# Kernel tuning notes

Measured on AMD Instinct MI355X. Metric: run time of the kernel, lower is better.

Reference implementation:

```python
import jax, jax.numpy as jnp
import numpy as np

N = 100000      # nodes
E = 1600000     # edges (avg degree 16)
F_IN = 128      # node feature dim
HID = 128       # conv1 out
EMB = 64        # conv2 out (embedding)
OUT = 40        # classes


def setup_inputs() -> dict:
    key = jax.random.key(0)
    ks = jax.random.split(key, 8)
    x = jax.random.normal(ks[0], (N, F_IN), dtype=jnp.float32)
    edge_index = jax.random.randint(ks[1], (2, E), 0, N, dtype=jnp.int64)

    def glorot(k, shape):
        lim = np.sqrt(6.0 / (shape[0] + shape[1])).astype(np.float32)
        return jax.random.uniform(k, shape, jnp.float32, -lim, lim)

    W1 = glorot(ks[2], (F_IN, HID)); b1 = jnp.zeros((HID,), jnp.float32)
    W2 = glorot(ks[3], (HID, EMB)); b2 = jnp.zeros((EMB,), jnp.float32)
    Wl = glorot(ks[4], (EMB, OUT)); bl = jnp.zeros((OUT,), jnp.float32)
    return {"x": x, "edge_index": edge_index,
            "W1": W1, "b1": b1, "W2": W2, "b2": b2, "Wl": Wl, "bl": bl}


def _gcn_conv(x, W, b, src, dst, norm, n):
    # GCNConv: linear transform first (smaller width earlier), then normalized
    # sparse aggregation: out_i = sum_{j->i} norm_e * (x_j W) + b
    h = x @ W
    out = jax.ops.segment_sum(h[src] * norm[:, None], dst, num_segments=n)
    return out + b


def reference(x, edge_index, W1, b1, W2, b2, Wl, bl):
    n = x.shape[0]
    loop = jnp.arange(n, dtype=edge_index.dtype)
    # add self loops (GCNConv default)
    src = jnp.concatenate([edge_index[0], loop])
    dst = jnp.concatenate([edge_index[1], loop])
    # symmetric degree normalization: D^{-1/2} (A+I) D^{-1/2}
    deg = jax.ops.segment_sum(jnp.ones_like(dst, x.dtype), dst, num_segments=n)
    dinv = jnp.where(deg > 0, jax.lax.rsqrt(deg), 0.0)
    norm = dinv[src] * dinv[dst]

    h = jax.nn.relu(_gcn_conv(x, W1, b1, src, dst, norm, n))
    # F.dropout(training=False) is identity in eval mode
    embedding = _gcn_conv(h, W2, b2, src, dst, norm, n)
    logits = embedding @ Wl + bl
    return jax.nn.log_softmax(logits, axis=1), embedding
```

## Files before the change

kernel.cpp:

```cpp
#include <hip/hip_runtime.h>
#include <math.h>

#define F_IN 128
#define HIDN 128
#define EMBD 64
#define OUTC 40

#define NBINS 1024
#define BIN_SHIFT 7
#define CSR_BLKS 256

__host__ __device__ static inline int imin(int a, int b) { return a < b ? a : b; }

typedef __attribute__((ext_vector_type(8))) short s16x8;
typedef __attribute__((ext_vector_type(4))) float f32x4;

__device__ __forceinline__ unsigned short f2bf(float f) {
    unsigned int u = __builtin_bit_cast(unsigned int, f);
    u = (u + 0x7FFFu + ((u >> 16) & 1u)) >> 16;
    return (unsigned short)u;
}
__device__ __forceinline__ float bflo(unsigned int v) {
    return __builtin_bit_cast(float, v << 16);
}
__device__ __forceinline__ float bfhi(unsigned int v) {
    return __builtin_bit_cast(float, v & 0xFFFF0000u);
}

__host__ __device__ static inline int csr_chunk(int E) {
    return (((E + CSR_BLKS - 1) / CSR_BLKS) + 3) & ~3;
}

__global__ __launch_bounds__(256) void prep_frags_kernel(
    const float* __restrict__ W1, const float* __restrict__ W2,
    const float* __restrict__ Wl, unsigned short* __restrict__ W1f,
    unsigned short* __restrict__ W2f, unsigned short* __restrict__ Wlf) {
    int s = blockIdx.x * 256 + threadIdx.x;
    if (s < 2048) {
        int lane = s & 63, r = s >> 6;
        int ks = r & 3, cf = (r >> 2) & 3, wcol = r >> 4;
        int c = wcol * 64 + cf * 16 + (lane & 15);
        int kb = ks * 32 + (lane >> 4) * 8;
        unsigned short* d = W1f + s * 8;
#pragma unroll
        for (int j = 0; j < 8; ++j) d[j] = f2bf(W1[(size_t)(kb + j) * HIDN + c]);
    } else if (s < 3072) {
        int q = s - 2048;
        int lane = q & 63, r = q >> 6;
        int ks = r & 3, wv = r >> 2;
        int c = wv * 16 + (lane & 15);
        int kb = ks * 32 + (lane >> 4) * 8;
        unsigned short* d = W2f + q * 8;
#pragma unroll
        for (int j = 0; j < 8; ++j) d[j] = f2bf(W2[(size_t)(kb + j) * EMBD + c]);
    } else if (s < 3456) {
        int q = s - 3072;
        int lane = q & 63, r = q >> 6;
        int ks = r & 1, ct = r >> 1;
        int c = ct * 16 + (lane & 15);
        int kb = ks * 32 + (lane >> 4) * 8;
        unsigned short* d = Wlf + q * 8;
#pragma unroll
        for (int j = 0; j < 8; ++j)
            d[j] = (c < OUTC) ? f2bf(Wl[(size_t)(kb + j) * OUTC + c]) : (unsigned short)0;
    }
}

__global__ __launch_bounds__(256) void coarse_hist_kernel(const int* __restrict__ dst,
                                                          int* __restrict__ bc, int E) {
    __shared__ int h[NBINS];
    for (int i = threadIdx.x; i < NBINS; i += 256) h[i] = 0;
    __syncthreads();
    const int chunk = csr_chunk(E);
    const int e0 = blockIdx.x * chunk;
    const int e1 = imin(e0 + chunk, E);
    for (int e = e0 + threadIdx.x; e < e1; e += 256)
        atomicAdd(&h[dst[e] >> BIN_SHIFT], 1);
    __syncthreads();
    for (int i = threadIdx.x; i < NBINS; i += 256)
        bc[blockIdx.x * NBINS + i] = h[i];
}

__global__ __launch_bounds__(64) void bin_prefix_kernel(int* __restrict__ bc,
                                                        int* __restrict__ bintot) {
    const int bin = blockIdx.x * 64 + threadIdx.x;
    int run = 0;
    for (int blk = 0; blk < CSR_BLKS; ++blk) {
        int v = bc[blk * NBINS + bin];
        bc[blk * NBINS + bin] = run;
        run += v;
    }
    bintot[bin] = run;
}

__global__ __launch_bounds__(1024) void bin_scan_kernel(const int* __restrict__ bintot,
                                                        int* __restrict__ cs) {
    __shared__ int s[NBINS];
    const int t = threadIdx.x;
    s[t] = bintot[t];
    __syncthreads();
    for (int off = 1; off < NBINS; off <<= 1) {
        int v = (t >= off) ? s[t - off] : 0;
        __syncthreads();
        s[t] += v;
        __syncthreads();
    }
    cs[t + 1] = s[t];
    if (t == 0) cs[0] = 0;
}

__global__ __launch_bounds__(256) void bin_scatter_kernel(const int* __restrict__ src,
                                                          const int* __restrict__ dst,
                                                          const int* __restrict__ bc,
                                                          const int* __restrict__ cs,
                                                          int* __restrict__ ebuf, int E) {
    __shared__ int cur[NBINS];
    for (int i = threadIdx.x; i < NBINS; i += 256)
        cur[i] = cs[i] + bc[blockIdx.x * NBINS + i];
    __syncthreads();
    const int chunk = csr_chunk(E);
    const int e0 = blockIdx.x * chunk;
    const int e1 = imin(e0 + chunk, E);
    int e = e0 + threadIdx.x * 4;
    for (; e + 3 < e1; e += 256 * 4) {
        int4 d = *(const int4*)(dst + e);
        int4 s = *(const int4*)(src + e);
        int p0 = atomicAdd(&cur[d.x >> BIN_SHIFT], 1);
        int p1 = atomicAdd(&cur[d.y >> BIN_SHIFT], 1);
        int p2 = atomicAdd(&cur[d.z >> BIN_SHIFT], 1);
        int p3 = atomicAdd(&cur[d.w >> BIN_SHIFT], 1);
        ebuf[p0] = (s.x << BIN_SHIFT) | (d.x & 127);
        ebuf[p1] = (s.y << BIN_SHIFT) | (d.y & 127);
        ebuf[p2] = (s.z << BIN_SHIFT) | (d.z & 127);
        ebuf[p3] = (s.w << BIN_SHIFT) | (d.w & 127);
    }
    for (; e < e1; ++e) {
        int d = dst[e];
        int pos = atomicAdd(&cur[d >> BIN_SHIFT], 1);
        ebuf[pos] = (src[e] << BIN_SHIFT) | (d & 127);
    }
}

__global__ __launch_bounds__(256) void fine_build_kernel(const int* __restrict__ ebuf,
                                                         const int* __restrict__ cs,
                                                         int* __restrict__ degi,
                                                         int* __restrict__ rowptr,
                                                         float* __restrict__ dinv,
                                                         int* __restrict__ col, int n) {
    __shared__ int h[128];
    __shared__ int fs[128];
    __shared__ int cur[128];
    const int b = blockIdx.x;
    const int node0 = b << BIN_SHIFT;
    const int t = threadIdx.x;
    if (t < 128) h[t] = 0;
    __syncthreads();
    const int e0 = cs[b], e1 = cs[b + 1];
    for (int e = e0 + t; e < e1; e += 256)
        atomicAdd(&h[ebuf[e] & 127], 1);
    __syncthreads();
    if (t < 128) fs[t] = h[t];
    __syncthreads();
    for (int off = 1; off < 128; off <<= 1) {
        int v = 0;
        if (t < 128 && t >= off) v = fs[t - off];
        __syncthreads();
        if (t < 128) fs[t] += v;
        __syncthreads();
    }
    if (t < 128) {
        int node = node0 + t;
        if (node < n) {
            int cnt = h[t];
            degi[node] = cnt;
            rowptr[node] = e0 + fs[t] - cnt;
            dinv[node] = rsqrtf((float)cnt + 1.0f);
        }
        cur[t] = 0;
    }
    __syncthreads();
    for (int e = e0 + t; e < e1; e += 256) {
        int p = ebuf[e];
        int li = p & 127;
        int loc = atomicAdd(&cur[li], 1);
        col[e0 + (fs[li] - h[li]) + loc] = p >> BIN_SHIFT;
    }
}

template <typename InT, int K, int M, int WM, int WN>
__global__ __launch_bounds__(256) void gemm_mfma_kernel(const InT* __restrict__ X,
                                                        const unsigned short* __restrict__ Wfrag,
                                                        const float* __restrict__ dinv,
                                                        unsigned short* __restrict__ Y,
                                                        int n, int ntiles) {
    constexpr int BM = 64;
    constexpr int WR = BM / WM;
    constexpr int WC = M / WN;
    constexpr int RF = WR / 16;
    constexpr int CF = WC / 16;
    constexpr int KS = K / 32;
    constexpr int ROWB = K * 2;
    constexpr int UPR = ROWB / 16;

    __shared__ char Xs[BM * ROWB];

    const int tid = threadIdx.x;
    const int lane = tid & 63;
    const int wid = tid >> 6;
    const int wrow = wid / WN;
    const int wcol = wid % WN;
    const int l15 = lane & 15;
    const int lhi = lane >> 4;

    s16x8 bfrag[CF][KS];
#pragma unroll
    for (int cf = 0; cf < CF; ++cf)
#pragma unroll
        for (int ks = 0; ks < KS; ++ks)
            bfrag[cf][ks] = *(const s16x8*)(Wfrag +
                (size_t)(((wcol * CF + cf) * KS + ks) * 64 + lane) * 8);

    for (int tile = blockIdx.x; tile < ntiles; tile += gridDim.x) {
        const int row0 = tile * BM;
        __syncthreads();
#pragma unroll
        for (int i = 0; i < (BM * UPR) / 256; ++i) {
            int g = i * 256 + tid;
            int r = g / UPR, u = g % UPR;
            int grow = row0 + r;
            int4 val = make_int4(0, 0, 0, 0);
            if (grow < n) {
                if constexpr (sizeof(InT) == 4) {
                    const float* src = (const float*)X + (size_t)grow * K + u * 8;
                    float4 f0 = *(const float4*)src;
                    float4 f1 = *(const float4*)(src + 4);
                    val.x = (int)(f2bf(f0.x) | ((unsigned int)f2bf(f0.y) << 16));
                    val.y = (int)(f2bf(f0.z) | ((unsigned int)f2bf(f0.w) << 16));
                    val.z = (int)(f2bf(f1.x) | ((unsigned int)f2bf(f1.y) << 16));
                    val.w = (int)(f2bf(f1.z) | ((unsigned int)f2bf(f1.w) << 16));
                } else {
                    val = *(const int4*)((const unsigned short*)X + (size_t)grow * K + u * 8);
                }
            }
            *(int4*)(Xs + r * ROWB + ((u ^ (r & 7)) * 16)) = val;
        }
        __syncthreads();

        f32x4 acc[RF][CF];
#pragma unroll
        for (int rf = 0; rf < RF; ++rf)
#pragma unroll
            for (int cf = 0; cf < CF; ++cf) acc[rf][cf] = (f32x4)(0.0f);
#pragma unroll
        for (int ks = 0; ks < KS; ++ks) {
            s16x8 afrag[RF];
#pragma unroll
            for (int rf = 0; rf < RF; ++rf) {
                int r = wrow * WR + rf * 16 + l15;
                int u = ks * 4 + lhi;
                afrag[rf] = *(const s16x8*)(Xs + r * ROWB + ((u ^ (r & 7)) * 16));
            }
#pragma unroll
            for (int rf = 0; rf < RF; ++rf)
#pragma unroll
                for (int cf = 0; cf < CF; ++cf)
                    acc[rf][cf] = __builtin_amdgcn_mfma_f32_16x16x32_bf16(
                        afrag[rf], bfrag[cf][ks], acc[rf][cf], 0, 0, 0);
        }

#pragma unroll
        for (int rf = 0; rf < RF; ++rf) {
#pragma unroll
            for (int reg = 0; reg < 4; ++reg) {
                int grow = row0 + wrow * WR + rf * 16 + lhi * 4 + reg;
                if (grow < n) {
                    float dv = dinv[grow];
#pragma unroll
                    for (int cf = 0; cf < CF; ++cf) {
                        int colg = wcol * WC + cf * 16 + l15;
                        Y[(size_t)grow * M + colg] = f2bf(acc[rf][cf][reg] * dv);
                    }
                }
            }
        }
    }
}

__global__ __launch_bounds__(256) void gather_gemm_kernel(
    const unsigned short* __restrict__ Hs1, const int* __restrict__ rowptr,
    const int* __restrict__ degi, const int* __restrict__ col,
    const float* __restrict__ dinv, const float* __restrict__ b1,
    const unsigned short* __restrict__ W2f, unsigned short* __restrict__ Hs2, int n) {
    __shared__ char h_tile[16 * 256];

    const int tid = threadIdx.x;
    const int lane = tid & 63;
    const int wv = tid >> 6;
    const int sub = lane & 15;
    const int grp = lane >> 4;
    const int node0 = blockIdx.x * 16;
    const int local = wv * 4 + grp;
    const int node = node0 + local;
    const int foff = sub * 8;

    s16x8 bfrag[4];
#pragma unroll
    for (int ks = 0; ks < 4; ++ks)
        bfrag[ks] = *(const s16x8*)(W2f + (size_t)((wv * 4 + ks) * 64 + lane) * 8);

    if (node < n) {
        const int start = rowptr[node];
        const int cnt = degi[node];
        const float dvn = dinv[node];
        float acc[8];
        {
            int4 v = *(const int4*)(Hs1 + (size_t)node * HIDN + foff);
#pragma unroll
            for (int q = 0; q < 4; ++q) {
                unsigned int w = ((const unsigned int*)&v)[q];
                acc[2 * q] = bflo(w);
                acc[2 * q + 1] = bfhi(w);
            }
        }
        int m0 = imin(cnt, 16);
        int sv = (sub < m0) ? col[start + sub] : 0;
        for (int base = 0; base < cnt; base += 16) {
            int m = imin(cnt - base, 16);
            int svn = 0;
            int nb = base + 16;
            if (nb < cnt) {
                int mn = imin(cnt - nb, 16);
                svn = (sub < mn) ? col[start + nb + sub] : 0;
            }
            int k = 0;
            for (; k + 8 <= m; k += 8) {
                int4 a[8];
#pragma unroll
                for (int j = 0; j < 8; ++j) {
                    int s = __shfl(sv, k + j, 16);
                    a[j] = *(const int4*)(Hs1 + (size_t)s * HIDN + foff);
                }
#pragma unroll
                for (int j = 0; j < 8; ++j)
#pragma unroll
                    for (int q = 0; q < 4; ++q) {
                        unsigned int w = ((const unsigned int*)&a[j])[q];
                        acc[2 * q] += bflo(w);
                        acc[2 * q + 1] += bfhi(w);
                    }
            }
            for (; k + 2 <= m; k += 2) {
                int s0 = __shfl(sv, k, 16);
                int s1 = __shfl(sv, k + 1, 16);
                int4 a0 = *(const int4*)(Hs1 + (size_t)s0 * HIDN + foff);
                int4 a1 = *(const int4*)(Hs1 + (size_t)s1 * HIDN + foff);
#pragma unroll
                for (int q = 0; q < 4; ++q) {
                    unsigned int w0 = ((const unsigned int*)&a0)[q];
                    unsigned int w1 = ((const unsigned int*)&a1)[q];
                    acc[2 * q] += bflo(w0);
                    acc[2 * q + 1] += bfhi(w0);
                    acc[2 * q] += bflo(w1);
                    acc[2 * q + 1] += bfhi(w1);
                }
            }
            for (; k < m; ++k) {
                int s = __shfl(sv, k, 16);
                int4 a = *(const int4*)(Hs1 + (size_t)s * HIDN + foff);
#pragma unroll
                for (int q = 0; q < 4; ++q) {
                    unsigned int w = ((const unsigned int*)&a)[q];
                    acc[2 * q] += bflo(w);
                    acc[2 * q + 1] += bfhi(w);
                }
            }
            sv = svn;
        }
        float4 bv0 = *(const float4*)(b1 + foff);
        float4 bv1 = *(const float4*)(b1 + foff + 4);
        float o[8];
        o[0] = fmaxf(dvn * acc[0] + bv0.x, 0.f);
        o[1] = fmaxf(dvn * acc[1] + bv0.y, 0.f);
        o[2] = fmaxf(dvn * acc[2] + bv0.z, 0.f);
        o[3] = fmaxf(dvn * acc[3] + bv0.w, 0.f);
        o[4] = fmaxf(dvn * acc[4] + bv1.x, 0.f);
        o[5] = fmaxf(dvn * acc[5] + bv1.y, 0.f);
        o[6] = fmaxf(dvn * acc[6] + bv1.z, 0.f);
        o[7] = fmaxf(dvn * acc[7] + bv1.w, 0.f);
        int4 p;
        ((unsigned int*)&p)[0] = f2bf(o[0]) | ((unsigned int)f2bf(o[1]) << 16);
        ((unsigned int*)&p)[1] = f2bf(o[2]) | ((unsigned int)f2bf(o[3]) << 16);
        ((unsigned int*)&p)[2] = f2bf(o[4]) | ((unsigned int)f2bf(o[5]) << 16);
        ((unsigned int*)&p)[3] = f2bf(o[6]) | ((unsigned int)f2bf(o[7]) << 16);
        *(int4*)(h_tile + local * 256 + ((sub ^ (local & 7)) * 16)) = p;
    }
    __syncthreads();

    f32x4 acc2 = (f32x4)(0.0f);
#pragma unroll
    for (int ks = 0; ks < 4; ++ks) {
        int r = sub;
        int u = ks * 4 + grp;
        s16x8 af = *(const s16x8*)(h_tile + r * 256 + ((u ^ (r & 7)) * 16));
        acc2 = __builtin_amdgcn_mfma_f32_16x16x32_bf16(af, bfrag[ks], acc2, 0, 0, 0);
    }
#pragma unroll
    for (int reg = 0; reg < 4; ++reg) {
        int row = grp * 4 + reg;
        int nd = node0 + row;
        if (nd < n)
            Hs2[(size_t)nd * EMBD + wv * 16 + sub] = f2bf(acc2[reg] * dinv[nd]);
    }
}

__global__ __launch_bounds__(256) void gather2_lsm_kernel(
    const unsigned short* __restrict__ Hs, const int* __restrict__ rowptr,
    const int* __restrict__ degi, const int* __restrict__ col,
    const float* __restrict__ dinv, const float* __restrict__ b2,
    const unsigned short* __restrict__ Wlf, const float* __restrict__ bl,
    float* __restrict__ emb, float* __restrict__ lsm, int n) {
    __shared__ char h_tile[32 * 128];
    __shared__ float lg[32][49];
    __shared__ float bls[OUTC];

    const int tid = threadIdx.x;
    if (tid < OUTC) bls[tid] = bl[tid];
    const int lane = tid & 63;
    const int wv = tid >> 6;
    const int sub = lane & 7;
    const int grp = lane >> 3;
    const int local = wv * 8 + grp;
    const int node0 = blockIdx.x * 32;
    const int node = node0 + local;
    const int foff = sub * 8;

    if (node < n) {
        const int start = rowptr[node];
        const int cnt = degi[node];
        const float dvn = dinv[node];
        float acc[8];
        {
            int4 v = *(const int4*)(Hs + (size_t)node * EMBD + foff);
#pragma unroll
            for (int q = 0; q < 4; ++q) {
                unsigned int w = ((const unsigned int*)&v)[q];
                acc[2 * q] = bflo(w);
                acc[2 * q + 1] = bfhi(w);
            }
        }
        int m0 = imin(cnt, 8);
        int sv = (sub < m0) ? col[start + sub] : 0;
        for (int base = 0; base < cnt; base += 8) {
            int m = imin(cnt - base, 8);
            int svn = 0;
            int nb = base + 8;
            if (nb < cnt) {
                int mn = imin(cnt - nb, 8);
                svn = (sub < mn) ? col[start + nb + sub] : 0;
            }
            int k = 0;
            for (; k + 8 <= m; k += 8) {
                int4 a[8];
#pragma unroll
                for (int j = 0; j < 8; ++j) {
                    int s = __shfl(sv, k + j, 8);
                    a[j] = *(const int4*)(Hs + (size_t)s * EMBD + foff);
                }
#pragma unroll
                for (int j = 0; j < 8; ++j)
#pragma unroll
                    for (int q = 0; q < 4; ++q) {
                        unsigned int w = ((const unsigned int*)&a[j])[q];
                        acc[2 * q] += bflo(w);
                        acc[2 * q + 1] += bfhi(w);
                    }
            }
            for (; k < m; ++k) {
                int s = __shfl(sv, k, 8);
                int4 a = *(const int4*)(Hs + (size_t)s * EMBD + foff);
#pragma unroll
                for (int q = 0; q < 4; ++q) {
                    unsigned int w = ((const unsigned int*)&a)[q];
                    acc[2 * q] += bflo(w);
                    acc[2 * q + 1] += bfhi(w);
                }
            }
            sv = svn;
        }

        float4 bv0 = *(const float4*)(b2 + foff);
        float4 bv1 = *(const float4*)(b2 + foff + 4);
        float o[8];
        o[0] = dvn * acc[0] + bv0.x; o[1] = dvn * acc[1] + bv0.y;
        o[2] = dvn * acc[2] + bv0.z; o[3] = dvn * acc[3] + bv0.w;
        o[4] = dvn * acc[4] + bv1.x; o[5] = dvn * acc[5] + bv1.y;
        o[6] = dvn * acc[6] + bv1.z; o[7] = dvn * acc[7] + bv1.w;
        *(float4*)(emb + (size_t)node * EMBD + foff) = make_float4(o[0], o[1], o[2], o[3]);
        *(float4*)(emb + (size_t)node * EMBD + foff + 4) = make_float4(o[4], o[5], o[6], o[7]);
        int4 p;
        ((unsigned int*)&p)[0] = f2bf(o[0]) | ((unsigned int)f2bf(o[1]) << 16);
        ((unsigned int*)&p)[1] = f2bf(o[2]) | ((unsigned int)f2bf(o[3]) << 16);
        ((unsigned int*)&p)[2] = f2bf(o[4]) | ((unsigned int)f2bf(o[5]) << 16);
        ((unsigned int*)&p)[3] = f2bf(o[6]) | ((unsigned int)f2bf(o[7]) << 16);
        *(int4*)(h_tile + local * 128 + ((sub ^ (local & 7)) * 16)) = p;
    }
    __syncthreads();

    const int l15 = lane & 15;
    const int lhi = lane >> 4;
#pragma unroll
    for (int it = 0; it < 2; ++it) {
        int t = wv + it * 4;
        if (t < 6) {
            int rt = t & 1, ct = t >> 1;
            f32x4 accl = (f32x4)(0.0f);
#pragma unroll
            for (int ks = 0; ks < 2; ++ks) {
                int r = rt * 16 + l15;
                int u = ks * 4 + lhi;
                s16x8 af = *(const s16x8*)(h_tile + r * 128 + ((u ^ (r & 7)) * 16));
                s16x8 bf = *(const s16x8*)(Wlf + (size_t)((ct * 2 + ks) * 64 + lane) * 8);
                accl = __builtin_amdgcn_mfma_f32_16x16x32_bf16(af, bf, accl, 0, 0, 0);
            }
#pragma unroll
            for (int reg = 0; reg < 4; ++reg)
                lg[rt * 16 + lhi * 4 + reg][ct * 16 + l15] = accl[reg];
        }
    }
    __syncthreads();

    if (tid < 32) {
        int nd = node0 + tid;
        if (nd < n) {
            float logit[OUTC];
            float mx = -INFINITY;
#pragma unroll
            for (int c = 0; c < OUTC; ++c) {
                float v = lg[tid][c] + bls[c];
                logit[c] = v;
                mx = fmaxf(mx, v);
            }
            float ss = 0.0f;
#pragma unroll
            for (int c = 0; c < OUTC; ++c) ss += expf(logit[c] - mx);
            float lse = mx + logf(ss);
            float* op = lsm + (size_t)nd * OUTC;
#pragma unroll
            for (int c = 0; c < OUTC; ++c) op[c] = logit[c] - lse;
        }
    }
}

extern "C" void kernel_launch(void* const* d_in, const int* in_sizes, int n_in,
                              void* d_out, int out_size, void* d_ws, size_t ws_size,
                              hipStream_t stream) {
    const float* x  = (const float*)d_in[0];
    const int*   ei = (const int*)d_in[1];
    const float* W1 = (const float*)d_in[2];
    const float* b1 = (const float*)d_in[3];
    const float* W2 = (const float*)d_in[4];
    const float* b2 = (const float*)d_in[5];
    const float* Wl = (const float*)d_in[6];
    const float* bl = (const float*)d_in[7];

    const int N = in_sizes[0] / F_IN;
    const int E = in_sizes[1] / 2;
    const int* srcp = ei;
    const int* dstp = ei + E;

    float* out = (float*)d_out;
    float* lsm = out;
    float* emb = out + (size_t)N * OUTC;

    float* ws    = (float*)d_ws;
    float* dinv  = ws;
    int*   degi  = (int*)(ws + N);
    int*   rowptr= degi + N;
    int*   cs    = rowptr + N;
    int*   bintot= cs + 1056;
    int*   bc    = bintot + NBINS;
    unsigned short* W1f = (unsigned short*)(bc + CSR_BLKS * NBINS);
    unsigned short* W2f = W1f + 16384;
    unsigned short* Wlf = W2f + 8192;
    int*   col   = (int*)(Wlf + 3072);
    int*   ebuf  = col + E;
    unsigned short* Hs1 = (unsigned short*)(ebuf + E);
    unsigned short* Hs2 = Hs1 + (size_t)N * HIDN;

    const int B = 256;
    const int ntiles = (N + 63) / 64;

    prep_frags_kernel<<<14, B, 0, stream>>>(W1, W2, Wl, W1f, W2f, Wlf);

    coarse_hist_kernel<<<CSR_BLKS, B, 0, stream>>>(dstp, bc, E);
    bin_prefix_kernel<<<NBINS / 64, 64, 0, stream>>>(bc, bintot);
    bin_scan_kernel<<<1, 1024, 0, stream>>>(bintot, cs);
    bin_scatter_kernel<<<CSR_BLKS, B, 0, stream>>>(srcp, dstp, bc, cs, ebuf, E);
    fine_build_kernel<<<(N + 127) / 128, B, 0, stream>>>(ebuf, cs, degi, rowptr, dinv, col, N);

    gemm_mfma_kernel<float, F_IN, HIDN, 2, 2><<<784, B, 0, stream>>>(x, W1f, dinv, Hs1, N, ntiles);

    gather_gemm_kernel<<<(N + 15) / 16, B, 0, stream>>>(
        Hs1, rowptr, degi, col, dinv, b1, W2f, Hs2, N);

    gather2_lsm_kernel<<<(N + 31) / 32, B, 0, stream>>>(
        Hs2, rowptr, degi, col, dinv, b2, Wlf, bl, emb, lsm, N);
}
```

Baseline: 190.9 us.

## Sort nodes by degree within bins to balance gather workload

Builds a per-128-node permutation in fine_build_kernel that orders nodes by in-degree. Both aggregation kernels then process nodes in that order, so lanes and warps in a block see similar neighbour counts. The coarse histogram is also vectorised with int4 loads, and the first GEMM grid is sized to the tile count. The permutation adds an indirection and makes output writes less contiguous.

```diff
diff --git a/kernel.cpp b/kernel.cpp
--- a/kernel.cpp
+++ b/kernel.cpp
@@ -74,8 +74,15 @@
     const int chunk = csr_chunk(E);
     const int e0 = blockIdx.x * chunk;
     const int e1 = imin(e0 + chunk, E);
-    for (int e = e0 + threadIdx.x; e < e1; e += 256)
-        atomicAdd(&h[dst[e] >> BIN_SHIFT], 1);
+    int e = e0 + threadIdx.x * 4;
+    for (; e + 3 < e1; e += 256 * 4) {
+        int4 d = *(const int4*)(dst + e);
+        atomicAdd(&h[d.x >> BIN_SHIFT], 1);
+        atomicAdd(&h[d.y >> BIN_SHIFT], 1);
+        atomicAdd(&h[d.z >> BIN_SHIFT], 1);
+        atomicAdd(&h[d.w >> BIN_SHIFT], 1);
+    }
+    for (; e < e1; ++e) atomicAdd(&h[dst[e] >> BIN_SHIFT], 1);
     __syncthreads();
     for (int i = threadIdx.x; i < NBINS; i += 256)
         bc[blockIdx.x * NBINS + i] = h[i];
@@ -146,7 +153,8 @@
                                                          int* __restrict__ degi,
                                                          int* __restrict__ rowptr,
                                                          float* __restrict__ dinv,
-                                                         int* __restrict__ col, int n) {
+                                                         int* __restrict__ col,
+                                                         int* __restrict__ perm, int n) {
     __shared__ int h[128];
     __shared__ int fs[128];
     __shared__ int cur[128];
@@ -184,6 +192,31 @@
         int li = p & 127;
         int loc = atomicAdd(&cur[li], 1);
         col[e0 + (fs[li] - h[li]) + loc] = p >> BIN_SHIFT;
+    }
+    __syncthreads();
+    if (t < 128) cur[t] = 0;
+    __syncthreads();
+    int mydeg = 0;
+    const bool valid = (t < 128) && (node0 + t < n);
+    if (valid) {
+        mydeg = imin(h[t], 127);
+        atomicAdd(&cur[mydeg], 1);
+    }
+    __syncthreads();
+    if (t < 128) fs[t] = cur[t];
+    __syncthreads();
+    for (int off = 1; off < 128; off <<= 1) {
+        int v = 0;
+        if (t < 128 && t >= off) v = fs[t - off];
+        __syncthreads();
+        if (t < 128) fs[t] += v;
+        __syncthreads();
+    }
+    if (t < 128) cur[t] = fs[t] - cur[t];
+    __syncthreads();
+    if (valid) {
+        int r = atomicAdd(&cur[mydeg], 1);
+        perm[node0 + r] = node0 + t;
     }
 }
 
@@ -290,8 +323,10 @@
     const unsigned short* __restrict__ Hs1, const int* __restrict__ rowptr,
     const int* __restrict__ degi, const int* __restrict__ col,
     const float* __restrict__ dinv, const float* __restrict__ b1,
-    const unsigned short* __restrict__ W2f, unsigned short* __restrict__ Hs2, int n) {
+    const unsigned short* __restrict__ W2f, const int* __restrict__ perm,
+    unsigned short* __restrict__ Hs2, int n) {
     __shared__ char h_tile[16 * 256];
+    __shared__ int nodes[16];
 
     const int tid = threadIdx.x;
     const int lane = tid & 63;
@@ -300,7 +335,9 @@
     const int grp = lane >> 4;
     const int node0 = blockIdx.x * 16;
     const int local = wv * 4 + grp;
-    const int node = node0 + local;
+    const int idx = node0 + local;
+    const int node = (idx < n) ? perm[idx] : -1;
+    if (tid < 16) nodes[tid] = (node0 + tid < n) ? perm[node0 + tid] : -1;
     const int foff = sub * 8;
 
     s16x8 bfrag[4];
@@ -308,7 +345,7 @@
     for (int ks = 0; ks < 4; ++ks)
         bfrag[ks] = *(const s16x8*)(W2f + (size_t)((wv * 4 + ks) * 64 + lane) * 8);
 
-    if (node < n) {
+    if (node >= 0) {
         const int start = rowptr[node];
         const int cnt = degi[node];
         const float dvn = dinv[node];
@@ -407,8 +444,8 @@
 #pragma unroll
     for (int reg = 0; reg < 4; ++reg) {
         int row = grp * 4 + reg;
-        int nd = node0 + row;
-        if (nd < n)
+        int nd = nodes[row];
+        if (nd >= 0)
             Hs2[(size_t)nd * EMBD + wv * 16 + sub] = f2bf(acc2[reg] * dinv[nd]);
     }
 }
@@ -418,7 +455,8 @@
     const int* __restrict__ degi, const int* __restrict__ col,
     const float* __restrict__ dinv, const float* __restrict__ b2,
     const unsigned short* __restrict__ Wlf, const float* __restrict__ bl,
-    float* __restrict__ emb, float* __restrict__ lsm, int n) {
+    const int* __restrict__ perm, float* __restrict__ emb,
+    float* __restrict__ lsm, int n) {
     __shared__ char h_tile[32 * 128];
     __shared__ float lg[32][49];
     __shared__ float bls[OUTC];
@@ -431,10 +469,11 @@
     const int grp = lane >> 3;
     const int local = wv * 8 + grp;
     const int node0 = blockIdx.x * 32;
-    const int node = node0 + local;
+    const int idx = node0 + local;
+    const int node = (idx < n) ? perm[idx] : -1;
     const int foff = sub * 8;
 
-    if (node < n) {
+    if (node >= 0) {
         const int start = rowptr[node];
         const int cnt = degi[node];
         const float dvn = dinv[node];
@@ -530,8 +569,9 @@
     __syncthreads();
 
     if (tid < 32) {
-        int nd = node0 + tid;
-        if (nd < n) {
+        int idx2 = node0 + tid;
+        if (idx2 < n) {
+            int nd = perm[idx2];
             float logit[OUTC];
             float mx = -INFINITY;
 #pragma unroll
@@ -576,7 +616,8 @@
     float* dinv  = ws;
     int*   degi  = (int*)(ws + N);
     int*   rowptr= degi + N;
-    int*   cs    = rowptr + N;
+    int*   perm  = rowptr + N;
+    int*   cs    = perm + N + 128;
     int*   bintot= cs + 1056;
     int*   bc    = bintot + NBINS;
     unsigned short* W1f = (unsigned short*)(bc + CSR_BLKS * NBINS);
@@ -596,13 +637,14 @@
     bin_prefix_kernel<<<NBINS / 64, 64, 0, stream>>>(bc, bintot);
     bin_scan_kernel<<<1, 1024, 0, stream>>>(bintot, cs);
     bin_scatter_kernel<<<CSR_BLKS, B, 0, stream>>>(srcp, dstp, bc, cs, ebuf, E);
-    fine_build_kernel<<<(N + 127) / 128, B, 0, stream>>>(ebuf, cs, degi, rowptr, dinv, col, N);
-
-    gemm_mfma_kernel<float, F_IN, HIDN, 2, 2><<<784, B, 0, stream>>>(x, W1f, dinv, Hs1, N, ntiles);
+    fine_build_kernel<<<(N + 127) / 128, B, 0, stream>>>(ebuf, cs, degi, rowptr, dinv,
+                                                         col, perm, N);
+
+    gemm_mfma_kernel<float, F_IN, HIDN, 2, 2><<<ntiles, B, 0, stream>>>(x, W1f, dinv, Hs1, N, ntiles);
 
     gather_gemm_kernel<<<(N + 15) / 16, B, 0, stream>>>(
-        Hs1, rowptr, degi, col, dinv, b1, W2f, Hs2, N);
+        Hs1, rowptr, degi, col, dinv, b1, W2f, perm, Hs2, N);
 
     gather2_lsm_kernel<<<(N + 31) / 32, B, 0, stream>>>(
-        Hs2, rowptr, degi, col, dinv, b2, Wlf, bl, emb, lsm, N);
-}
+        Hs2, rowptr, degi, col, dinv, b2, Wlf, bl, perm, emb, lsm, N);
+}
```

Result: slower. 195.5 us (+2.4%).
